# Optimization experiments

Hardware: AMD Instinct MI355X
Metric: run time of the kernel (lower is better)

The kernel has to match this reference:

```python
import jax, jax.numpy as jnp
import numpy as np

WS = 8  # window size
NH = 8  # num heads
LN_EPS = 1e-5


def _rel_pos_index(ws):
    coords = np.stack(np.meshgrid(np.arange(ws), np.arange(ws), indexing='ij'))  # [2,ws,ws]
    cf = coords.reshape(2, -1)                      # [2, ws*ws]
    rc = (cf[:, :, None] - cf[:, None, :]).transpose(1, 2, 0).astype(np.int64)  # [N,N,2]
    rc[..., 0] += ws - 1
    rc[..., 1] += ws - 1
    rc[..., 0] *= 2 * ws - 1
    return jnp.asarray(rc.sum(-1), dtype=jnp.int32)  # [N,N]


def setup_inputs() -> dict:
    key = jax.random.key(0)
    B, C, H, W = 8, 256, 128, 128
    hid = 4 * C
    ks = jax.random.split(key, 16)
    rn = lambda k, shape, s=0.02: (jax.random.normal(k, shape, jnp.float32) * s)
    return {
        'x': jax.random.normal(ks[0], (B, H * W, C), jnp.float32),
        'feature': jax.random.normal(ks[1], (B, C, H, W), jnp.float32),
        'Wq': rn(ks[2], (C, C)), 'bq': jnp.zeros((C,), jnp.float32),
        'Wk': rn(ks[3], (C, C)), 'bk': jnp.zeros((C,), jnp.float32),
        'Wv': rn(ks[4], (C, C)), 'bv': jnp.zeros((C,), jnp.float32),
        'Wo': rn(ks[5], (C, C)), 'bo': jnp.zeros((C,), jnp.float32),
        'rpb_table': rn(ks[6], ((2 * WS - 1) ** 2, NH)),
        'g1': jnp.ones((C,), jnp.float32), 'beta1': jnp.zeros((C,), jnp.float32),
        'g2': jnp.ones((C,), jnp.float32), 'beta2': jnp.zeros((C,), jnp.float32),
        'Wm1': rn(ks[7], (C, hid)), 'bm1': jnp.zeros((hid,), jnp.float32),
        'Wm2': rn(ks[8], (hid, C)), 'bm2': jnp.zeros((C,), jnp.float32),
        'Wu1': rn(ks[9], (C, C)), 'bu1': jnp.zeros((C,), jnp.float32),
        'Wu2': rn(ks[10], (C, C)), 'bu2': jnp.zeros((C,), jnp.float32),
        'rel_idx': _rel_pos_index(WS),
    }


def _gelu(t):
    return jax.nn.gelu(t, approximate=False)  # torch nn.GELU default (erf)


def _ln(t, g, b):
    mu = jnp.mean(t, axis=-1, keepdims=True)
    var = jnp.var(t, axis=-1, keepdims=True)
    return (t - mu) * jax.lax.rsqrt(var + LN_EPS) * g + b


def reference(x, feature, Wq, bq, Wk, bk, Wv, bv, Wo, bo, rpb_table,
              g1, beta1, g2, beta2, Wm1, bm1, Wm2, bm2, Wu1, bu1, Wu2, bu2,
              rel_idx):
    B, C, H, W = feature.shape
    ws, nh = WS, NH
    hd = C // nh
    scale = hd ** -0.5

    # unary potential: Linear -> GELU -> Linear on x [B, HW, C]
    unary = _gelu(x @ Wu1 + bu1) @ Wu2 + bu2

    # window partition of feature
    f = feature.reshape(B, C, H * W).transpose(0, 2, 1)  # [B, HW, C]
    pad_h = (-H) % ws
    pad_w = (-W) % ws
    fimg = f.reshape(B, H, W, C)
    if pad_h or pad_w:
        fimg = jnp.pad(fimg, ((0, 0), (0, pad_h), (0, pad_w), (0, 0)))
    Hp, Wp_ = H + pad_h, W + pad_w
    win = fimg.reshape(B, Hp // ws, ws, Wp_ // ws, ws, C)
    win = win.transpose(0, 1, 3, 2, 4, 5).reshape(-1, ws * ws, C)  # [nW, N, C]

    xn = _ln(win, g1, beta1)
    N = ws * ws
    q = (xn @ Wq + bq).reshape(-1, N, nh, hd).transpose(0, 2, 1, 3)  # [nW, h, N, d]
    k = (xn @ Wk + bk).reshape(-1, N, nh, hd).transpose(0, 2, 1, 3)
    v = (xn @ Wv + bv).reshape(-1, N, nh, hd).transpose(0, 2, 1, 3)

    attn = jnp.einsum('whnd,whmd->whnm', q, k) * scale
    bias = rpb_table[rel_idx.reshape(-1)].reshape(N, N, nh).transpose(2, 0, 1)  # [h,N,N]
    attn = jax.nn.softmax(attn + bias[None], axis=-1)
    o = jnp.einsum('whnm,whmd->whnd', attn, v)
    o = o.transpose(0, 2, 1, 3).reshape(-1, N, C) @ Wo + bo  # [nW, N, C]

    # window reverse
    rev = o.reshape(B, Hp // ws, Wp_ // ws, ws, ws, C)
    rev = rev.transpose(0, 1, 3, 2, 4, 5).reshape(B, Hp, Wp_, C)
    if pad_h or pad_w:
        rev = rev[:, :H, :W, :]
    rev = rev.reshape(B, H * W, C)

    x2 = unary + rev
    out = x2 + (_gelu(_ln(x2, g2, beta2) @ Wm1 + bm1) @ Wm2 + bm2)
    return out
```

## Files before the change

### kernel.cpp

```cpp
#include <hip/hip_runtime.h>
#include <cmath>


typedef unsigned short u16;
typedef unsigned int u32;
typedef __bf16 bf16x8 __attribute__((ext_vector_type(8)));
typedef float f32x4 __attribute__((ext_vector_type(4)));

#define EPI_NONE 0
#define EPI_GELU 1
#define EPI_ADD 3

#define MTOK 131072
#define CC 256
#define HWC 16384

__device__ __forceinline__ float b2f(u16 u) {
    union { u32 i; float f; } x; x.i = ((u32)u) << 16; return x.f;
}
__device__ __forceinline__ u16 f2b(float f) {
    union { float f; u32 i; } x; x.f = f;
    u32 r = x.i + 0x7fffu + ((x.i >> 16) & 1u);
    return (u16)(r >> 16);
}
__device__ __forceinline__ u32 cvtpk(float lo, float hi) {
    u32 r;
    asm("v_cvt_pk_bf16_f32 %0, %1, %2" : "=v"(r) : "v"(lo), "v"(hi));
    return r;
}
__device__ __forceinline__ float gelu_f(float v) {
    return 0.5f * v * (1.0f + erff(v * 0.7071067811865475f));
}

__global__ __launch_bounds__(256) void cvt_f32_bf16(
    const float* __restrict__ src, u16* __restrict__ dst, long n)
{
    long i = ((long)blockIdx.x * 256 + threadIdx.x) * 8;
    if (i >= n) return;
    float4 a = *(const float4*)(src + i);
    float4 b = *(const float4*)(src + i + 4);
    union { uint4 v; u16 u[8]; } o;
    o.u[0] = f2b(a.x); o.u[1] = f2b(a.y); o.u[2] = f2b(a.z); o.u[3] = f2b(a.w);
    o.u[4] = f2b(b.x); o.u[5] = f2b(b.y); o.u[6] = f2b(b.z); o.u[7] = f2b(b.w);
    *(uint4*)(dst + i) = o.v;
}

__global__ __launch_bounds__(256) void transpose_f32_bf16(
    const float* __restrict__ src, u16* __restrict__ dst, int K, int N)
{
    __shared__ float t[32][33];
    const int k0 = blockIdx.x * 32, n0 = blockIdx.y * 32;
    const int tx = threadIdx.x & 31, ty = threadIdx.x >> 5;
    for (int i = ty; i < 32; i += 8)
        t[i][tx] = src[(long)(k0 + i) * N + n0 + tx];
    __syncthreads();
    for (int i = ty; i < 32; i += 8)
        dst[(long)(n0 + i) * K + k0 + tx] = f2b(t[tx][i]);
}

__global__ __launch_bounds__(256) void rpb_gather(
    const float* __restrict__ rpb, const int* __restrict__ rel, float* __restrict__ outb)
{
    int e = blockIdx.x * 256 + threadIdx.x;
    int h = e >> 12, idx = e & 4095;
    int mi = idx >> 10, ni = (idx >> 8) & 3, lane = (idx >> 2) & 63, r = idx & 3;
    int row = mi * 16 + (lane >> 4) * 4 + r;
    int tok = 4 * (lane & 15) + ni;
    outb[e] = 1.4426950408889634f * rpb[rel[row * 64 + tok] * 8 + h];
}

__global__ __launch_bounds__(256) void ln_stats(
    const float* __restrict__ feat, float* __restrict__ muP, float* __restrict__ rsP)
{
    __shared__ float red1[4][256];
    __shared__ float red2[4][256];
    const int blk = blockIdx.x;
    const int b = blk >> 6, h2 = blk & 63;
    const int t = threadIdx.x;
    const int c_off = t >> 6, lane = t & 63;
    const int rl = lane >> 5, w4 = (lane & 31) * 4;
    const int tok0 = rl * 128 + w4;
    const float* fp = feat + (long)b * 256 * HWC + (long)(h2 * 2 + rl) * 128 + w4;
    float s1[4] = {0.f, 0.f, 0.f, 0.f};
    float s2[4] = {0.f, 0.f, 0.f, 0.f};
#pragma unroll 4
    for (int it = 0; it < 64; it++) {
        int c = it * 4 + c_off;
        float4 f = *(const float4*)(fp + (long)c * HWC);
        s1[0] += f.x; s2[0] += f.x * f.x;
        s1[1] += f.y; s2[1] += f.y * f.y;
        s1[2] += f.z; s2[2] += f.z * f.z;
        s1[3] += f.w; s2[3] += f.w * f.w;
    }
    *(float4*)&red1[c_off][tok0] = *(float4*)s1;
    *(float4*)&red2[c_off][tok0] = *(float4*)s2;
    __syncthreads();
    float a = red1[0][t] + red1[1][t] + red1[2][t] + red1[3][t];
    float q = red2[0][t] + red2[1][t] + red2[2][t] + red2[3][t];
    float mu = a * (1.f / 256.f);
    float var = q * (1.f / 256.f) - mu * mu;
    long tg = (long)b * HWC + h2 * 256 + t;
    muP[tg] = mu;
    rsP[tg] = rsqrtf(var + 1e-5f);
}

__global__ __launch_bounds__(256) void ln_transpose(
    const float* __restrict__ feat, const float* __restrict__ muP,
    const float* __restrict__ rsP, const float* __restrict__ g1,
    const float* __restrict__ be1, u16* __restrict__ xn)
{
    __shared__ u16 ct[64 * 258];
    const int blk = blockIdx.x;
    const int b = blk >> 6, h2 = blk & 63;
    const int t = threadIdx.x;
    const int c_off = t >> 6, lane = t & 63;
    const int rl = lane >> 5, w4 = (lane & 31) * 4;
    const int tok0 = rl * 128 + w4;
    const long tokg0 = (long)b * HWC + h2 * 256;
    const float4 mu4 = *(const float4*)(muP + tokg0 + tok0);
    const float4 rs4 = *(const float4*)(rsP + tokg0 + tok0);
    const float* fp = feat + (long)b * 256 * HWC + (long)(h2 * 2 + rl) * 128 + w4;
    const int koff = t & 3;

    for (int ch = 0; ch < 4; ch++) {
#pragma unroll
        for (int it = 0; it < 16; it++) {
            int c = ch * 64 + it * 4 + c_off;
            float4 f = *(const float4*)(fp + (long)c * HWC);
            float gg = g1[c], bb = be1[c];
            float v0 = (f.x - mu4.x) * rs4.x * gg + bb;
            float v1 = (f.y - mu4.y) * rs4.y * gg + bb;
            float v2 = (f.z - mu4.z) * rs4.z * gg + bb;
            float v3 = (f.w - mu4.w) * rs4.w * gg + bb;
            uint2 pk;
            pk.x = cvtpk(v0, v1);
            pk.y = cvtpk(v2, v3);
            *(uint2*)&ct[(it * 4 + c_off) * 258 + tok0] = pk;
        }
        __syncthreads();
#pragma unroll
        for (int p = 0; p < 4; p++) {
            int token = p * 64 + (t >> 2);
            union { uint4 q[2]; u16 u[16]; } pkk;
#pragma unroll
            for (int cc = 0; cc < 16; cc++)
                pkk.u[cc] = ct[(koff * 16 + cc) * 258 + token];
            u16* op = xn + (tokg0 + token) * 256 + ch * 64 + koff * 16;
            *(uint4*)(op) = pkk.q[0];
            *(uint4*)(op + 8) = pkk.q[1];
        }
        __syncthreads();
    }
}

__global__ __launch_bounds__(256) void ln_rows(
    const u16* __restrict__ x, const float* __restrict__ g2,
    const float* __restrict__ be2, u16* __restrict__ out)
{
    const int wave = threadIdx.x >> 6, lane = threadIdx.x & 63;
    const long row = (long)blockIdx.x * 4 + wave;
    union { uint2 v; u16 u[4]; } pk;
    pk.v = *(const uint2*)(x + row * 256 + lane * 4);
    float v0 = b2f(pk.u[0]), v1 = b2f(pk.u[1]), v2 = b2f(pk.u[2]), v3 = b2f(pk.u[3]);
    float s1 = v0 + v1 + v2 + v3;
    float s2 = v0 * v0 + v1 * v1 + v2 * v2 + v3 * v3;
    for (int off = 1; off < 64; off <<= 1) {
        s1 += __shfl_xor(s1, off);
        s2 += __shfl_xor(s2, off);
    }
    float mu = s1 * (1.f / 256.f);
    float var = s2 * (1.f / 256.f) - mu * mu;
    float rs = rsqrtf(var + 1e-5f);
    float4 go = *(const float4*)(g2 + lane * 4);
    float4 bo2 = *(const float4*)(be2 + lane * 4);
    union { uint2 v; u16 u[4]; } ot;
    ot.u[0] = f2b((v0 - mu) * rs * go.x + bo2.x);
    ot.u[1] = f2b((v1 - mu) * rs * go.y + bo2.y);
    ot.u[2] = f2b((v2 - mu) * rs * go.z + bo2.z);
    ot.u[3] = f2b((v3 - mu) * rs * go.w + bo2.w);
    *(uint2*)(out + row * 256 + lane * 4) = ot.v;
}

template <int EPI, bool OUTF32>
__global__ __launch_bounds__(256) void gemm_bt(
    const u16* __restrict__ A, const u16* __restrict__ BT,
    const float* __restrict__ bias, void* __restrict__ outv,
    const u16* __restrict__ res, int M, int N, int K)
{
    __shared__ u16 As[128 * 32];
    __shared__ u16 Bs[128 * 32];
    const int tid = threadIdx.x;
    const int m0 = blockIdx.x * 128;
    const int n0 = blockIdx.y * 128;
    const int wave = tid >> 6, lane = tid & 63;
    const int wm = wave >> 1, wn = wave & 1;
    const int quad = lane >> 4, l16 = lane & 15;

    f32x4 acc[4][4];
#pragma unroll
    for (int i = 0; i < 4; i++)
#pragma unroll
        for (int j = 0; j < 4; j++) acc[i][j] = (f32x4){0.f, 0.f, 0.f, 0.f};

    const int srow = wave * 32 + (lane >> 2);
    const int scol = (lane & 3) * 8;
    const u16* gA = A + (long)(m0 + srow) * K + scol;
    const u16* gB = BT + (long)(n0 + srow) * K + scol;
    u16* lA = &As[srow * 32 + scol];
    u16* lB = &Bs[srow * 32 + scol];

    for (int k0 = 0; k0 < K; k0 += 32) {
        __syncthreads();
        __builtin_amdgcn_global_load_lds(
            (const __attribute__((address_space(1))) void*)(gA + k0),
            (__attribute__((address_space(3))) void*)lA, 16, 0, 0);
        __builtin_amdgcn_global_load_lds(
            (const __attribute__((address_space(1))) void*)(gA + k0 + 16 * K),
            (__attribute__((address_space(3))) void*)(lA + 16 * 32), 16, 0, 0);
        __builtin_amdgcn_global_load_lds(
            (const __attribute__((address_space(1))) void*)(gB + k0),
            (__attribute__((address_space(3))) void*)lB, 16, 0, 0);
        __builtin_amdgcn_global_load_lds(
            (const __attribute__((address_space(1))) void*)(gB + k0 + 16 * K),
            (__attribute__((address_space(3))) void*)(lB + 16 * 32), 16, 0, 0);
        __syncthreads();
        bf16x8 af[4], bfr[4];
#pragma unroll
        for (int mi = 0; mi < 4; mi++)
            af[mi] = *(const bf16x8*)&As[(wm * 64 + mi * 16 + l16) * 32 + quad * 8];
#pragma unroll
        for (int ni = 0; ni < 4; ni++)
            bfr[ni] = *(const bf16x8*)&Bs[(wn * 64 + ni * 16 + l16) * 32 + quad * 8];
#pragma unroll
        for (int mi = 0; mi < 4; mi++)
#pragma unroll
            for (int ni = 0; ni < 4; ni++)
                acc[mi][ni] = __builtin_amdgcn_mfma_f32_16x16x32_bf16(
                    bfr[ni], af[mi], acc[mi][ni], 0, 0, 0);
    }

#pragma unroll
    for (int mi = 0; mi < 4; mi++) {
        const int row = m0 + wm * 64 + mi * 16 + l16;
        const long rb = (long)row * N;
#pragma unroll
        for (int ni = 0; ni < 4; ni++) {
            const int cb = n0 + wn * 64 + ni * 16 + quad * 4;
            float4 bb = *(const float4*)(bias + cb);
            float v0 = acc[mi][ni][0] + bb.x;
            float v1 = acc[mi][ni][1] + bb.y;
            float v2 = acc[mi][ni][2] + bb.z;
            float v3 = acc[mi][ni][3] + bb.w;
            if constexpr (EPI == EPI_GELU) {
                v0 = gelu_f(v0); v1 = gelu_f(v1);
                v2 = gelu_f(v2); v3 = gelu_f(v3);
            }
            if constexpr (EPI == EPI_ADD) {
                uint2 rr = *(const uint2*)(res + rb + cb);
                v0 += b2f((u16)(rr.x & 0xffff));
                v1 += b2f((u16)(rr.x >> 16));
                v2 += b2f((u16)(rr.y & 0xffff));
                v3 += b2f((u16)(rr.y >> 16));
            }
            if constexpr (OUTF32) {
                float4 o = {v0, v1, v2, v3};
                *(float4*)((float*)outv + rb + cb) = o;
            } else {
                uint2 o;
                o.x = cvtpk(v0, v1);
                o.y = cvtpk(v2, v3);
                *(uint2*)((u16*)outv + rb + cb) = o;
            }
        }
    }
}

__device__ __forceinline__ long toff(int n) {
    return (long)((n >> 3) * 32768 + (n & 7) * 256);
}

__global__ __launch_bounds__(256, 3) void attn_kernel(
    const u16* __restrict__ qb, const u16* __restrict__ kb,
    const u16* __restrict__ vb, const float* __restrict__ biasp,
    u16* __restrict__ ob)
{
    __shared__ u16 lds[4 * 6400];
    const int wave = threadIdx.x >> 6, lane = threadIdx.x & 63;
    const int quad = lane >> 4, l16 = lane & 15;
    const int wid = blockIdx.x >> 1;
    const int h = ((blockIdx.x & 1) << 2) + wave;
    const int bI = wid >> 8, wh = (wid >> 4) & 15, ww = wid & 15;
    u16* Pl = lds + wave * 6400;
    u16* VT = Pl + 4096;
    const long base = ((long)bI * HWC + (wh * 8) * 128 + ww * 8) * 256 + h * 32;

    bf16x8 aq[4], bk4[4];
#pragma unroll
    for (int mi = 0; mi < 4; mi++)
        aq[mi] = *(const bf16x8*)(qb + base + toff(mi * 16 + l16) + quad * 8);
#pragma unroll
    for (int ni = 0; ni < 4; ni++)
        bk4[ni] = *(const bf16x8*)(kb + base + toff(4 * l16 + ni) + quad * 8);

    {
        const int t = lane;
        const int s = ((t >> 4) & 1) * 32 + ((t >> 2) & 3) * 8 + (t >> 5) * 4 + (t & 3);
        const u16* vp = vb + base + toff(t);
        union { uint4 v; u16 u[8]; } p0, p1, p2, p3;
        p0.v = *(const uint4*)(vp);
        p1.v = *(const uint4*)(vp + 8);
        p2.v = *(const uint4*)(vp + 16);
        p3.v = *(const uint4*)(vp + 24);
#pragma unroll
        for (int j = 0; j < 8; j++) {
            VT[j * 72 + s]        = p0.u[j];
            VT[(8 + j) * 72 + s]  = p1.u[j];
            VT[(16 + j) * 72 + s] = p2.u[j];
            VT[(24 + j) * 72 + s] = p3.u[j];
        }
    }

    f32x4 s[4][4];
#pragma unroll
    for (int i = 0; i < 4; i++)
#pragma unroll
        for (int j = 0; j < 4; j++) s[i][j] = (f32x4){0.f, 0.f, 0.f, 0.f};
    __builtin_amdgcn_s_setprio(1);
#pragma unroll
    for (int mi = 0; mi < 4; mi++)
#pragma unroll
        for (int ni = 0; ni < 4; ni++)
            s[mi][ni] = __builtin_amdgcn_mfma_f32_16x16x32_bf16(aq[mi], bk4[ni], s[mi][ni], 0, 0, 0);
    __builtin_amdgcn_s_setprio(0);

    const float* bp = biasp + h * 4096;
    const float SC2 = 0.17677669529663687f * 1.4426950408889634f;
    const int pq = l16 & 3, pks = (l16 >> 2) & 1, ph = l16 >> 3;
#pragma unroll
    for (int mi = 0; mi < 4; mi++) {
        f32x4 bb[4];
#pragma unroll
        for (int ni = 0; ni < 4; ni++)
            bb[ni] = *(const f32x4*)(bp + ((mi * 4 + ni) << 8) + lane * 4);
#pragma unroll
        for (int r = 0; r < 4; r++) {
            float p[4];
#pragma unroll
            for (int ni = 0; ni < 4; ni++)
                p[ni] = __builtin_amdgcn_exp2f(s[mi][ni][r] * SC2 + bb[ni][r]);
            float sum = (p[0] + p[1]) + (p[2] + p[3]);
            for (int off = 1; off < 16; off <<= 1) sum += __shfl_xor(sum, off);
            float inv = __builtin_amdgcn_rcpf(sum);
            int mrow = mi * 16 + quad * 4 + r;
            uint2 w2;
            w2.x = cvtpk(p[0] * inv, p[1] * inv);
            w2.y = cvtpk(p[2] * inv, p[3] * inv);
            *(uint2*)&Pl[pks * 2048 + mrow * 32 + pq * 8 + ph * 4] = w2;
        }
    }

    f32x4 o4[2][4];
#pragma unroll
    for (int i = 0; i < 2; i++)
#pragma unroll
        for (int j = 0; j < 4; j++) o4[i][j] = (f32x4){0.f, 0.f, 0.f, 0.f};
#pragma unroll
    for (int ks = 0; ks < 2; ks++) {
        bf16x8 at[2], pb[4];
#pragma unroll
        for (int mi = 0; mi < 2; mi++)
            at[mi] = *(const bf16x8*)&VT[(mi * 16 + l16) * 72 + ks * 32 + quad * 8];
#pragma unroll
        for (int nt = 0; nt < 4; nt++)
            pb[nt] = *(const bf16x8*)&Pl[ks * 2048 + (nt * 16 + l16) * 32 + quad * 8];
        __builtin_amdgcn_s_setprio(1);
#pragma unroll
        for (int mi = 0; mi < 2; mi++)
#pragma unroll
            for (int nt = 0; nt < 4; nt++)
                o4[mi][nt] = __builtin_amdgcn_mfma_f32_16x16x32_bf16(at[mi], pb[nt], o4[mi][nt], 0, 0, 0);
        __builtin_amdgcn_s_setprio(0);
    }

#pragma unroll
    for (int nt = 0; nt < 4; nt++)
#pragma unroll
        for (int mi = 0; mi < 2; mi++) {
            uint2 w2;
            w2.x = cvtpk(o4[mi][nt][0], o4[mi][nt][1]);
            w2.y = cvtpk(o4[mi][nt][2], o4[mi][nt][3]);
            *(uint2*)(ob + base + toff(nt * 16 + l16) + mi * 16 + quad * 4) = w2;
        }
}

extern "C" void kernel_launch(void* const* d_in, const int* in_sizes, int n_in,
                              void* d_out, int out_size, void* d_ws, size_t ws_size,
                              hipStream_t stream)
{
    (void)in_sizes; (void)n_in; (void)out_size; (void)ws_size;
    const float* x    = (const float*)d_in[0];
    const float* feat = (const float*)d_in[1];
    const float* Wq = (const float*)d_in[2];   const float* bq = (const float*)d_in[3];
    const float* Wk = (const float*)d_in[4];   const float* bk = (const float*)d_in[5];
    const float* Wv = (const float*)d_in[6];   const float* bv = (const float*)d_in[7];
    const float* Wo = (const float*)d_in[8];   const float* bo = (const float*)d_in[9];
    const float* rpb = (const float*)d_in[10];
    const float* g1 = (const float*)d_in[11];  const float* be1 = (const float*)d_in[12];
    const float* g2 = (const float*)d_in[13];  const float* be2 = (const float*)d_in[14];
    const float* Wm1 = (const float*)d_in[15]; const float* bm1 = (const float*)d_in[16];
    const float* Wm2 = (const float*)d_in[17]; const float* bm2 = (const float*)d_in[18];
    const float* Wu1 = (const float*)d_in[19]; const float* bu1 = (const float*)d_in[20];
    const float* Wu2 = (const float*)d_in[21]; const float* bu2 = (const float*)d_in[22];
    const int* rel = (const int*)d_in[23];
    float* outp = (float*)d_out;

    char* ws = (char*)d_ws;
    u16* WqT  = (u16*)(ws);
    u16* WkT  = WqT + 65536;
    u16* WvT  = WkT + 65536;
    u16* WoT  = WvT + 65536;
    u16* Wu1T = WoT + 65536;
    u16* Wu2T = Wu1T + 65536;
    u16* Wm1T = Wu2T + 65536;
    u16* Wm2T = Wm1T + 262144;
    float* biasf = (float*)(ws + 1835008);
    const long MB = 1024L * 1024;
    u16* S0 = (u16*)(ws + 2 * MB);
    u16* S1 = (u16*)(ws + 66 * MB);
    u16* S2 = (u16*)(ws + 130 * MB);
    u16* xn  = (u16*)d_out;
    float* muP = (float*)((char*)d_out + 96 * MB);
    float* rsP = (float*)((char*)d_out + 97 * MB);
    u16* qb  = S0;
    u16* kb  = S1;
    u16* vb  = S2;
    u16* O   = S0;
    u16* xb  = S1;
    u16* u1h = S2;
    u16* un  = S1;
    u16* x2  = S2;
    u16* tch = S0;
    u16* hch = S1;

    const dim3 blk(256);

    transpose_f32_bf16<<<dim3(8, 8), blk, 0, stream>>>(Wq, WqT, 256, 256);
    transpose_f32_bf16<<<dim3(8, 8), blk, 0, stream>>>(Wk, WkT, 256, 256);
    transpose_f32_bf16<<<dim3(8, 8), blk, 0, stream>>>(Wv, WvT, 256, 256);
    transpose_f32_bf16<<<dim3(8, 8), blk, 0, stream>>>(Wo, WoT, 256, 256);
    transpose_f32_bf16<<<dim3(8, 8), blk, 0, stream>>>(Wu1, Wu1T, 256, 256);
    transpose_f32_bf16<<<dim3(8, 8), blk, 0, stream>>>(Wu2, Wu2T, 256, 256);
    transpose_f32_bf16<<<dim3(8, 32), blk, 0, stream>>>(Wm1, Wm1T, 256, 1024);
    transpose_f32_bf16<<<dim3(32, 8), blk, 0, stream>>>(Wm2, Wm2T, 1024, 256);
    rpb_gather<<<dim3(128), blk, 0, stream>>>(rpb, rel, biasf);

    ln_stats<<<dim3(512), blk, 0, stream>>>(feat, muP, rsP);
    ln_transpose<<<dim3(512), blk, 0, stream>>>(feat, muP, rsP, g1, be1, xn);

    gemm_bt<EPI_NONE, false><<<dim3(1024, 2), blk, 0, stream>>>(xn, WqT, bq, qb, nullptr, MTOK, 256, 256);
    gemm_bt<EPI_NONE, false><<<dim3(1024, 2), blk, 0, stream>>>(xn, WkT, bk, kb, nullptr, MTOK, 256, 256);
    gemm_bt<EPI_NONE, false><<<dim3(1024, 2), blk, 0, stream>>>(xn, WvT, bv, vb, nullptr, MTOK, 256, 256);

    attn_kernel<<<dim3(4096), blk, 0, stream>>>(qb, kb, vb, biasf, O);

    cvt_f32_bf16<<<dim3(16384), blk, 0, stream>>>(x, xb, (long)MTOK * 256);
    gemm_bt<EPI_GELU, false><<<dim3(1024, 2), blk, 0, stream>>>(xb, Wu1T, bu1, u1h, nullptr, MTOK, 256, 256);
    gemm_bt<EPI_NONE, false><<<dim3(1024, 2), blk, 0, stream>>>(u1h, Wu2T, bu2, un, nullptr, MTOK, 256, 256);

    gemm_bt<EPI_ADD, false><<<dim3(1024, 2), blk, 0, stream>>>(O, WoT, bo, x2, un, MTOK, 256, 256);

    for (int ch = 0; ch < 4; ch++) {
        const u16* x2c = x2 + (long)ch * 32768 * 256;
        float* outc = outp + (long)ch * 32768 * 256;
        ln_rows<<<dim3(8192), blk, 0, stream>>>(x2c, g2, be2, tch);
        gemm_bt<EPI_GELU, false><<<dim3(256, 8), blk, 0, stream>>>(tch, Wm1T, bm1, hch, nullptr, 32768, 1024, 256);
        gemm_bt<EPI_ADD, true><<<dim3(256, 2), blk, 0, stream>>>(hch, Wm2T, bm2, outc, x2c, 32768, 256, 1024);
    }
}
```

Measured before the change: 1.123 ms.

## Fold LN affine into weights, fuse QKV GEMM, and fuse input conversions into GEMMs

```diff
diff --git a/kernel.cpp b/kernel.cpp
--- a/kernel.cpp
+++ b/kernel.cpp
@@ -9,6 +9,7 @@
 
 #define EPI_NONE 0
 #define EPI_GELU 1
+#define EPI_WINREV 2
 #define EPI_ADD 3
 
 #define MTOK 131072
@@ -31,31 +32,37 @@
 __device__ __forceinline__ float gelu_f(float v) {
     return 0.5f * v * (1.0f + erff(v * 0.7071067811865475f));
 }
-
-__global__ __launch_bounds__(256) void cvt_f32_bf16(
-    const float* __restrict__ src, u16* __restrict__ dst, long n)
-{
-    long i = ((long)blockIdx.x * 256 + threadIdx.x) * 8;
-    if (i >= n) return;
-    float4 a = *(const float4*)(src + i);
-    float4 b = *(const float4*)(src + i + 4);
-    union { uint4 v; u16 u[8]; } o;
-    o.u[0] = f2b(a.x); o.u[1] = f2b(a.y); o.u[2] = f2b(a.z); o.u[3] = f2b(a.w);
-    o.u[4] = f2b(b.x); o.u[5] = f2b(b.y); o.u[6] = f2b(b.z); o.u[7] = f2b(b.w);
-    *(uint4*)(dst + i) = o.v;
+__device__ __forceinline__ u32 ln_word(u32 w, float rs, float nmurs) {
+    union { u32 i; float f; } lo, hi;
+    lo.i = w << 16; hi.i = w & 0xffff0000u;
+    return cvtpk(fmaf(lo.f, rs, nmurs), fmaf(hi.f, rs, nmurs));
 }
 
 __global__ __launch_bounds__(256) void transpose_f32_bf16(
-    const float* __restrict__ src, u16* __restrict__ dst, int K, int N)
+    const float* __restrict__ src, const float* __restrict__ scale,
+    u16* __restrict__ dst, int K, int N)
 {
     __shared__ float t[32][33];
     const int k0 = blockIdx.x * 32, n0 = blockIdx.y * 32;
     const int tx = threadIdx.x & 31, ty = threadIdx.x >> 5;
-    for (int i = ty; i < 32; i += 8)
-        t[i][tx] = src[(long)(k0 + i) * N + n0 + tx];
+    for (int i = ty; i < 32; i += 8) {
+        float sc = scale ? scale[k0 + i] : 1.0f;
+        t[i][tx] = src[(long)(k0 + i) * N + n0 + tx] * sc;
+    }
     __syncthreads();
     for (int i = ty; i < 32; i += 8)
         dst[(long)(n0 + i) * K + k0 + tx] = f2b(t[tx][i]);
+}
+
+__global__ __launch_bounds__(256) void bias_fold(
+    const float* __restrict__ W, const float* __restrict__ b,
+    const float* __restrict__ beta, float* __restrict__ out, int K, int N)
+{
+    int n = blockIdx.x * 256 + threadIdx.x;
+    if (n >= N) return;
+    float s = b[n];
+    for (int k = 0; k < K; k++) s += beta[k] * W[(long)k * N + n];
+    out[n] = s;
 }
 
 __global__ __launch_bounds__(256) void rpb_gather(
@@ -106,8 +113,7 @@
 
 __global__ __launch_bounds__(256) void ln_transpose(
     const float* __restrict__ feat, const float* __restrict__ muP,
-    const float* __restrict__ rsP, const float* __restrict__ g1,
-    const float* __restrict__ be1, u16* __restrict__ xn)
+    const float* __restrict__ rsP, u16* __restrict__ xn)
 {
     __shared__ u16 ct[64 * 258];
     const int blk = blockIdx.x;
@@ -127,25 +133,23 @@
         for (int it = 0; it < 16; it++) {
             int c = ch * 64 + it * 4 + c_off;
             float4 f = *(const float4*)(fp + (long)c * HWC);
-            float gg = g1[c], bb = be1[c];
-            float v0 = (f.x - mu4.x) * rs4.x * gg + bb;
-            float v1 = (f.y - mu4.y) * rs4.y * gg + bb;
-            float v2 = (f.z - mu4.z) * rs4.z * gg + bb;
-            float v3 = (f.w - mu4.w) * rs4.w * gg + bb;
             uint2 pk;
-            pk.x = cvtpk(v0, v1);
-            pk.y = cvtpk(v2, v3);
+            pk.x = cvtpk((f.x - mu4.x) * rs4.x, (f.y - mu4.y) * rs4.y);
+            pk.y = cvtpk((f.z - mu4.z) * rs4.z, (f.w - mu4.w) * rs4.w);
             *(uint2*)&ct[(it * 4 + c_off) * 258 + tok0] = pk;
         }
         __syncthreads();
 #pragma unroll
         for (int p = 0; p < 4; p++) {
             int token = p * 64 + (t >> 2);
+            int hh = h2 * 2 + (token >> 7), wc = token & 127;
+            long orow = ((long)b * 256 + (hh >> 3) * 16 + (wc >> 3)) * 64
+                      + (hh & 7) * 8 + (wc & 7);
             union { uint4 q[2]; u16 u[16]; } pkk;
 #pragma unroll
             for (int cc = 0; cc < 16; cc++)
                 pkk.u[cc] = ct[(koff * 16 + cc) * 258 + token];
-            u16* op = xn + (tokg0 + token) * 256 + ch * 64 + koff * 16;
+            u16* op = xn + orow * 256 + ch * 64 + koff * 16;
             *(uint4*)(op) = pkk.q[0];
             *(uint4*)(op + 8) = pkk.q[1];
         }
@@ -153,9 +157,8 @@
     }
 }
 
-__global__ __launch_bounds__(256) void ln_rows(
-    const u16* __restrict__ x, const float* __restrict__ g2,
-    const float* __restrict__ be2, u16* __restrict__ out)
+__global__ __launch_bounds__(256) void ln2_stats(
+    const u16* __restrict__ x, float* __restrict__ mu, float* __restrict__ rs)
 {
     const int wave = threadIdx.x >> 6, lane = threadIdx.x & 63;
     const long row = (long)blockIdx.x * 4 + wave;
@@ -168,30 +171,27 @@
         s1 += __shfl_xor(s1, off);
         s2 += __shfl_xor(s2, off);
     }
-    float mu = s1 * (1.f / 256.f);
-    float var = s2 * (1.f / 256.f) - mu * mu;
-    float rs = rsqrtf(var + 1e-5f);
-    float4 go = *(const float4*)(g2 + lane * 4);
-    float4 bo2 = *(const float4*)(be2 + lane * 4);
-    union { uint2 v; u16 u[4]; } ot;
-    ot.u[0] = f2b((v0 - mu) * rs * go.x + bo2.x);
-    ot.u[1] = f2b((v1 - mu) * rs * go.y + bo2.y);
-    ot.u[2] = f2b((v2 - mu) * rs * go.z + bo2.z);
-    ot.u[3] = f2b((v3 - mu) * rs * go.w + bo2.w);
-    *(uint2*)(out + row * 256 + lane * 4) = ot.v;
-}
-
-template <int EPI, bool OUTF32>
-__global__ __launch_bounds__(256) void gemm_bt(
-    const u16* __restrict__ A, const u16* __restrict__ BT,
-    const float* __restrict__ bias, void* __restrict__ outv,
-    const u16* __restrict__ res, int M, int N, int K)
+    if (lane == 0) {
+        float m = s1 * (1.f / 256.f);
+        float var = s2 * (1.f / 256.f) - m * m;
+        mu[row] = m;
+        rs[row] = rsqrtf(var + 1e-5f);
+    }
+}
+
+template <int EPI, bool OUTF32, int ASRC, bool SPLIT3>
+__global__ __launch_bounds__(256) void gemm_core(
+    const void* __restrict__ Av, const u16* __restrict__ BT,
+    const float* __restrict__ bias, void* __restrict__ out0,
+    void* __restrict__ out1, void* __restrict__ out2,
+    const u16* __restrict__ res, const float* __restrict__ muA,
+    const float* __restrict__ rsA, int M, int N, int K)
 {
     __shared__ u16 As[128 * 32];
     __shared__ u16 Bs[128 * 32];
     const int tid = threadIdx.x;
-    const int m0 = blockIdx.x * 128;
-    const int n0 = blockIdx.y * 128;
+    const int n0 = blockIdx.x * 128;
+    const int m0 = blockIdx.y * 128;
     const int wave = tid >> 6, lane = tid & 63;
     const int wm = wave >> 1, wn = wave & 1;
     const int quad = lane >> 4, l16 = lane & 15;
@@ -203,20 +203,69 @@
         for (int j = 0; j < 4; j++) acc[i][j] = (f32x4){0.f, 0.f, 0.f, 0.f};
 
     const int srow = wave * 32 + (lane >> 2);
-    const int scol = (lane & 3) * 8;
-    const u16* gA = A + (long)(m0 + srow) * K + scol;
-    const u16* gB = BT + (long)(n0 + srow) * K + scol;
-    u16* lA = &As[srow * 32 + scol];
-    u16* lB = &Bs[srow * 32 + scol];
+    const int gch = ((lane & 3) ^ ((lane >> 3) & 3)) * 8;
+    const u16* gB = BT + (long)(n0 + srow) * K + gch;
+    u16* lB = &Bs[srow * 32 + (lane & 3) * 8];
+
+    const u16* gA0 = nullptr; u16* lA = nullptr;
+    const float* gAf = nullptr; const u16* gAh = nullptr;
+    u16 *sA0 = nullptr, *sA1 = nullptr;
+    float rsv = 0.f, nmu = 0.f;
+    const int ar = tid >> 1;
+    const int aseg = (tid & 1) * 2;
+    const int ao = (tid >> 2) & 3;
+    if constexpr (ASRC == 0) {
+        gA0 = (const u16*)Av + (long)(m0 + srow) * K + gch;
+        lA = &As[srow * 32 + (lane & 3) * 8];
+    } else {
+        sA0 = &As[ar * 32 + (aseg ^ ao) * 8];
+        sA1 = &As[ar * 32 + ((aseg + 1) ^ ao) * 8];
+        if constexpr (ASRC == 1) {
+            gAf = (const float*)Av + (long)(m0 + ar) * K + aseg * 8;
+        } else {
+            gAh = (const u16*)Av + (long)(m0 + ar) * K + aseg * 8;
+            rsv = rsA[m0 + ar];
+            nmu = -muA[m0 + ar] * rsv;
+        }
+    }
+
+    const int rdsw = ((l16 >> 1) & 3);
 
     for (int k0 = 0; k0 < K; k0 += 32) {
+        float4 a0, a1, a2, a3;
+        uint4 u0, u1v;
+        if constexpr (ASRC == 1) {
+            a0 = *(const float4*)(gAf + k0);
+            a1 = *(const float4*)(gAf + k0 + 4);
+            a2 = *(const float4*)(gAf + k0 + 8);
+            a3 = *(const float4*)(gAf + k0 + 12);
+        } else if constexpr (ASRC == 2) {
+            u0 = *(const uint4*)(gAh + k0);
+            u1v = *(const uint4*)(gAh + k0 + 8);
+        }
         __syncthreads();
-        __builtin_amdgcn_global_load_lds(
-            (const __attribute__((address_space(1))) void*)(gA + k0),
-            (__attribute__((address_space(3))) void*)lA, 16, 0, 0);
-        __builtin_amdgcn_global_load_lds(
-            (const __attribute__((address_space(1))) void*)(gA + k0 + 16 * K),
-            (__attribute__((address_space(3))) void*)(lA + 16 * 32), 16, 0, 0);
+        if constexpr (ASRC == 0) {
+            __builtin_amdgcn_global_load_lds(
+                (const __attribute__((address_space(1))) void*)(gA0 + k0),
+                (__attribute__((address_space(3))) void*)lA, 16, 0, 0);
+            __builtin_amdgcn_global_load_lds(
+                (const __attribute__((address_space(1))) void*)(gA0 + k0 + 16 * K),
+                (__attribute__((address_space(3))) void*)(lA + 16 * 32), 16, 0, 0);
+        } else if constexpr (ASRC == 1) {
+            uint4 w0 = {cvtpk(a0.x, a0.y), cvtpk(a0.z, a0.w),
+                        cvtpk(a1.x, a1.y), cvtpk(a1.z, a1.w)};
+            uint4 w1 = {cvtpk(a2.x, a2.y), cvtpk(a2.z, a2.w),
+                        cvtpk(a3.x, a3.y), cvtpk(a3.z, a3.w)};
+            *(uint4*)sA0 = w0;
+            *(uint4*)sA1 = w1;
+        } else {
+            uint4 w0 = {ln_word(u0.x, rsv, nmu), ln_word(u0.y, rsv, nmu),
+                        ln_word(u0.z, rsv, nmu), ln_word(u0.w, rsv, nmu)};
+            uint4 w1 = {ln_word(u1v.x, rsv, nmu), ln_word(u1v.y, rsv, nmu),
+                        ln_word(u1v.z, rsv, nmu), ln_word(u1v.w, rsv, nmu)};
+            *(uint4*)sA0 = w0;
+            *(uint4*)sA1 = w1;
+        }
         __builtin_amdgcn_global_load_lds(
             (const __attribute__((address_space(1))) void*)(gB + k0),
             (__attribute__((address_space(3))) void*)lB, 16, 0, 0);
@@ -227,10 +276,10 @@
         bf16x8 af[4], bfr[4];
 #pragma unroll
         for (int mi = 0; mi < 4; mi++)
-            af[mi] = *(const bf16x8*)&As[(wm * 64 + mi * 16 + l16) * 32 + quad * 8];
+            af[mi] = *(const bf16x8*)&As[(wm * 64 + mi * 16 + l16) * 32 + ((quad ^ rdsw) * 8)];
 #pragma unroll
         for (int ni = 0; ni < 4; ni++)
-            bfr[ni] = *(const bf16x8*)&Bs[(wn * 64 + ni * 16 + l16) * 32 + quad * 8];
+            bfr[ni] = *(const bf16x8*)&Bs[(wn * 64 + ni * 16 + l16) * 32 + ((quad ^ rdsw) * 8)];
 #pragma unroll
         for (int mi = 0; mi < 4; mi++)
 #pragma unroll
@@ -242,7 +291,15 @@
 #pragma unroll
     for (int mi = 0; mi < 4; mi++) {
         const int row = m0 + wm * 64 + mi * 16 + l16;
-        const long rb = (long)row * N;
+        long orow;
+        if constexpr (EPI == EPI_WINREV) {
+            int wI = row >> 6, n = row & 63;
+            int bI = wI >> 8, rem = wI & 255;
+            int wh = rem >> 4, wwI = rem & 15;
+            orow = (long)bI * HWC + (long)((wh * 8 + (n >> 3)) * 128 + wwI * 8 + (n & 7));
+        } else {
+            orow = row;
+        }
 #pragma unroll
         for (int ni = 0; ni < 4; ni++) {
             const int cb = n0 + wn * 64 + ni * 16 + quad * 4;
@@ -255,28 +312,30 @@
                 v0 = gelu_f(v0); v1 = gelu_f(v1);
                 v2 = gelu_f(v2); v3 = gelu_f(v3);
             }
-            if constexpr (EPI == EPI_ADD) {
-                uint2 rr = *(const uint2*)(res + rb + cb);
+            if constexpr (EPI == EPI_WINREV || EPI == EPI_ADD) {
+                uint2 rr = *(const uint2*)(res + orow * (long)N + cb);
                 v0 += b2f((u16)(rr.x & 0xffff));
                 v1 += b2f((u16)(rr.x >> 16));
                 v2 += b2f((u16)(rr.y & 0xffff));
                 v3 += b2f((u16)(rr.y >> 16));
             }
-            if constexpr (OUTF32) {
+            if constexpr (SPLIT3) {
+                u16* ob = (u16*)(n0 < 256 ? out0 : n0 < 512 ? out1 : out2);
+                uint2 o;
+                o.x = cvtpk(v0, v1);
+                o.y = cvtpk(v2, v3);
+                *(uint2*)(ob + orow * 256L + (cb & 255)) = o;
+            } else if constexpr (OUTF32) {
                 float4 o = {v0, v1, v2, v3};
-                *(float4*)((float*)outv + rb + cb) = o;
+                *(float4*)((float*)out0 + orow * (long)N + cb) = o;
             } else {
                 uint2 o;
                 o.x = cvtpk(v0, v1);
                 o.y = cvtpk(v2, v3);
-                *(uint2*)((u16*)outv + rb + cb) = o;
+                *(uint2*)((u16*)out0 + orow * (long)N + cb) = o;
             }
         }
     }
-}
-
-__device__ __forceinline__ long toff(int n) {
-    return (long)((n >> 3) * 32768 + (n & 7) * 256);
 }
 
 __global__ __launch_bounds__(256, 3) void attn_kernel(
@@ -287,25 +346,24 @@
     __shared__ u16 lds[4 * 6400];
     const int wave = threadIdx.x >> 6, lane = threadIdx.x & 63;
     const int quad = lane >> 4, l16 = lane & 15;
-    const int wid = blockIdx.x >> 1;
+    const int w = blockIdx.x >> 1;
     const int h = ((blockIdx.x & 1) << 2) + wave;
-    const int bI = wid >> 8, wh = (wid >> 4) & 15, ww = wid & 15;
     u16* Pl = lds + wave * 6400;
     u16* VT = Pl + 4096;
-    const long base = ((long)bI * HWC + (wh * 8) * 128 + ww * 8) * 256 + h * 32;
+    const long base = (long)w * 64 * 256 + h * 32;
 
     bf16x8 aq[4], bk4[4];
 #pragma unroll
     for (int mi = 0; mi < 4; mi++)
-        aq[mi] = *(const bf16x8*)(qb + base + toff(mi * 16 + l16) + quad * 8);
+        aq[mi] = *(const bf16x8*)(qb + base + (long)(mi * 16 + l16) * 256 + quad * 8);
 #pragma unroll
     for (int ni = 0; ni < 4; ni++)
-        bk4[ni] = *(const bf16x8*)(kb + base + toff(4 * l16 + ni) + quad * 8);
+        bk4[ni] = *(const bf16x8*)(kb + base + (long)(4 * l16 + ni) * 256 + quad * 8);
 
     {
         const int t = lane;
         const int s = ((t >> 4) & 1) * 32 + ((t >> 2) & 3) * 8 + (t >> 5) * 4 + (t & 3);
-        const u16* vp = vb + base + toff(t);
+        const u16* vp = vb + base + (long)t * 256;
         union { uint4 v; u16 u[8]; } p0, p1, p2, p3;
         p0.v = *(const uint4*)(vp);
         p1.v = *(const uint4*)(vp + 8);
@@ -389,7 +447,7 @@
             uint2 w2;
             w2.x = cvtpk(o4[mi][nt][0], o4[mi][nt][1]);
             w2.y = cvtpk(o4[mi][nt][2], o4[mi][nt][3]);
-            *(uint2*)(ob + base + toff(nt * 16 + l16) + mi * 16 + quad * 4) = w2;
+            *(uint2*)(ob + base + (long)(nt * 16 + l16) * 256 + mi * 16 + quad * 4) = w2;
         }
 }
 
@@ -424,6 +482,8 @@
     u16* Wm1T = Wu2T + 65536;
     u16* Wm2T = Wm1T + 262144;
     float* biasf = (float*)(ws + 1835008);
+    float* bqkv  = (float*)(ws + 1966080);
+    float* bm1f  = (float*)(ws + 1970176);
     const long MB = 1024L * 1024;
     u16* S0 = (u16*)(ws + 2 * MB);
     u16* S1 = (u16*)(ws + 66 * MB);
@@ -435,45 +495,53 @@
     u16* kb  = S1;
     u16* vb  = S2;
     u16* O   = S0;
-    u16* xb  = S1;
     u16* u1h = S2;
     u16* un  = S1;
     u16* x2  = S2;
-    u16* tch = S0;
+    float* mu2 = (float*)S0;
+    float* rs2 = mu2 + MTOK;
     u16* hch = S1;
 
     const dim3 blk(256);
 
-    transpose_f32_bf16<<<dim3(8, 8), blk, 0, stream>>>(Wq, WqT, 256, 256);
-    transpose_f32_bf16<<<dim3(8, 8), blk, 0, stream>>>(Wk, WkT, 256, 256);
-    transpose_f32_bf16<<<dim3(8, 8), blk, 0, stream>>>(Wv, WvT, 256, 256);
-    transpose_f32_bf16<<<dim3(8, 8), blk, 0, stream>>>(Wo, WoT, 256, 256);
-    transpose_f32_bf16<<<dim3(8, 8), blk, 0, stream>>>(Wu1, Wu1T, 256, 256);
-    transpose_f32_bf16<<<dim3(8, 8), blk, 0, stream>>>(Wu2, Wu2T, 256, 256);
-    transpose_f32_bf16<<<dim3(8, 32), blk, 0, stream>>>(Wm1, Wm1T, 256, 1024);
-    transpose_f32_bf16<<<dim3(32, 8), blk, 0, stream>>>(Wm2, Wm2T, 1024, 256);
+    transpose_f32_bf16<<<dim3(8, 8), blk, 0, stream>>>(Wq, g1, WqT, 256, 256);
+    transpose_f32_bf16<<<dim3(8, 8), blk, 0, stream>>>(Wk, g1, WkT, 256, 256);
+    transpose_f32_bf16<<<dim3(8, 8), blk, 0, stream>>>(Wv, g1, WvT, 256, 256);
+    transpose_f32_bf16<<<dim3(8, 8), blk, 0, stream>>>(Wo, nullptr, WoT, 256, 256);
+    transpose_f32_bf16<<<dim3(8, 8), blk, 0, stream>>>(Wu1, nullptr, Wu1T, 256, 256);
+    transpose_f32_bf16<<<dim3(8, 8), blk, 0, stream>>>(Wu2, nullptr, Wu2T, 256, 256);
+    transpose_f32_bf16<<<dim3(8, 32), blk, 0, stream>>>(Wm1, g2, Wm1T, 256, 1024);
+    transpose_f32_bf16<<<dim3(32, 8), blk, 0, stream>>>(Wm2, nullptr, Wm2T, 1024, 256);
+    bias_fold<<<dim3(1), blk, 0, stream>>>(Wq, bq, be1, bqkv, 256, 256);
+    bias_fold<<<dim3(1), blk, 0, stream>>>(Wk, bk, be1, bqkv + 256, 256, 256);
+    bias_fold<<<dim3(1), blk, 0, stream>>>(Wv, bv, be1, bqkv + 512, 256, 256);
+    bias_fold<<<dim3(4), blk, 0, stream>>>(Wm1, bm1, be2, bm1f, 256, 1024);
     rpb_gather<<<dim3(128), blk, 0, stream>>>(rpb, rel, biasf);
 
     ln_stats<<<dim3(512), blk, 0, stream>>>(feat, muP, rsP);
-    ln_transpose<<<dim3(512), blk, 0, stream>>>(feat, muP, rsP, g1, be1, xn);
-
-    gemm_bt<EPI_NONE, false><<<dim3(1024, 2), blk, 0, stream>>>(xn, WqT, bq, qb, nullptr, MTOK, 256, 256);
-    gemm_bt<EPI_NONE, false><<<dim3(1024, 2), blk, 0, stream>>>(xn, WkT, bk, kb, nullptr, MTOK, 256, 256);
-    gemm_bt<EPI_NONE, false><<<dim3(1024, 2), blk, 0, stream>>>(xn, WvT, bv, vb, nullptr, MTOK, 256, 256);
+    ln_transpose<<<dim3(512), blk, 0, stream>>>(feat, muP, rsP, xn);
+
+    gemm_core<EPI_NONE, false, 0, true><<<dim3(6, 1024), blk, 0, stream>>>(
+        xn, WqT, bqkv, qb, kb, vb, nullptr, nullptr, nullptr, MTOK, 768, 256);
 
     attn_kernel<<<dim3(4096), blk, 0, stream>>>(qb, kb, vb, biasf, O);
 
-    cvt_f32_bf16<<<dim3(16384), blk, 0, stream>>>(x, xb, (long)MTOK * 256);
-    gemm_bt<EPI_GELU, false><<<dim3(1024, 2), blk, 0, stream>>>(xb, Wu1T, bu1, u1h, nullptr, MTOK, 256, 256);
-    gemm_bt<EPI_NONE, false><<<dim3(1024, 2), blk, 0, stream>>>(u1h, Wu2T, bu2, un, nullptr, MTOK, 256, 256);
-
-    gemm_bt<EPI_ADD, false><<<dim3(1024, 2), blk, 0, stream>>>(O, WoT, bo, x2, un, MTOK, 256, 256);
-
+    gemm_core<EPI_GELU, false, 1, false><<<dim3(2, 1024), blk, 0, stream>>>(
+        x, Wu1T, bu1, u1h, nullptr, nullptr, nullptr, nullptr, nullptr, MTOK, 256, 256);
+    gemm_core<EPI_NONE, false, 0, false><<<dim3(2, 1024), blk, 0, stream>>>(
+        u1h, Wu2T, bu2, un, nullptr, nullptr, nullptr, nullptr, nullptr, MTOK, 256, 256);
+
+    gemm_core<EPI_WINREV, false, 0, false><<<dim3(2, 1024), blk, 0, stream>>>(
+        O, WoT, bo, x2, nullptr, nullptr, un, nullptr, nullptr, MTOK, 256, 256);
+
+    ln2_stats<<<dim3(32768), blk, 0, stream>>>(x2, mu2, rs2);
     for (int ch = 0; ch < 4; ch++) {
         const u16* x2c = x2 + (long)ch * 32768 * 256;
         float* outc = outp + (long)ch * 32768 * 256;
-        ln_rows<<<dim3(8192), blk, 0, stream>>>(x2c, g2, be2, tch);
-        gemm_bt<EPI_GELU, false><<<dim3(256, 8), blk, 0, stream>>>(tch, Wm1T, bm1, hch, nullptr, 32768, 1024, 256);
-        gemm_bt<EPI_ADD, true><<<dim3(256, 2), blk, 0, stream>>>(hch, Wm2T, bm2, outc, x2c, 32768, 256, 1024);
-    }
-}
+        gemm_core<EPI_GELU, false, 2, false><<<dim3(8, 256), blk, 0, stream>>>(
+            x2c, Wm1T, bm1f, hch, nullptr, nullptr, nullptr,
+            mu2 + (long)ch * 32768, rs2 + (long)ch * 32768, 32768, 1024, 256);
+        gemm_core<EPI_ADD, true, 0, false><<<dim3(2, 256), blk, 0, stream>>>(
+            hch, Wm2T, bm2, outc, nullptr, nullptr, x2c, nullptr, nullptr, 32768, 256, 1024);
+    }
+}
```

Measured after the change: 1.353 ms. 1.21x slower.
